# Optimization experiments

Hardware: AMD Instinct MI355X
Metric: run time of the kernel (lower is better)

## Reference

```python
import jax, jax.numpy as jnp
import numpy as np

N = 4096      # nodes
IN = 512      # input_size
D = 128       # output_size per head
H = 4         # num_heads
SLOPE = 0.2   # leaky relu negative slope
NEG = -1e30   # masked-out logit value (finite to keep softmax grad-safe)


def setup_inputs() -> dict:
    key = jax.random.key(0)
    ks = jax.random.split(key, 8)
    stdv = 1.0 / np.sqrt(H * D)
    inputs = jax.random.normal(ks[0], (N, IN), jnp.float32)
    adjacency = jax.random.randint(ks[1], (N, N), 0, 2).astype(jnp.float32)  # dense 0/1 mask
    weight = jax.random.uniform(ks[2], (IN, H * D), jnp.float32, -stdv, stdv)
    weight_u = jax.random.uniform(ks[3], (H, D, 1), jnp.float32, -1.0, 1.0)
    weight_v = jax.random.uniform(ks[4], (H, D, 1), jnp.float32, -1.0, 1.0)
    bias = jax.random.uniform(ks[5], (1, H * D), jnp.float32, -stdv, stdv)
    proj_w = jax.random.normal(ks[6], (IN, H * D), jnp.float32) * 0.02
    proj_b = jnp.zeros((H * D,), jnp.float32)
    return {"inputs": inputs, "adjacency": adjacency, "weight": weight,
            "weight_u": weight_u, "weight_v": weight_v, "bias": bias,
            "proj_w": proj_w, "proj_b": proj_b}


def reference(inputs, adjacency, weight, weight_u, weight_v, bias, proj_w, proj_b):
    # support: [H, N, D]
    support = (inputs @ weight).reshape(N, H, D).transpose(1, 0, 2)
    # f1: per-source scores [H, 1, N]; f2: per-dest scores [H, N, 1]
    f1 = jnp.einsum('hnd,hdo->hn', support, weight_u)[:, None, :]
    f2 = jnp.einsum('hnd,hdo->hn', support, weight_v)[:, :, None]
    logits = f1 + f2                                  # [H, N, N]
    w = jnp.where(logits >= 0, logits, SLOPE * logits)  # leaky_relu
    masked = w * adjacency[None]                      # [H, N, N]
    # torch to_sparse keeps nonzero entries; sparse softmax treats the rest as -inf
    mask = masked != 0
    z = jnp.where(mask, masked, NEG)
    attn = jax.nn.softmax(z, axis=-1) * mask          # rows with no edges -> all zeros
    out = jnp.einsum('hij,hjd->hid', attn, support)   # [H, N, D]
    out = out.transpose(1, 0, 2).reshape(N, H * D)
    out = out + bias
    out = out + inputs @ proj_w + proj_b              # residual projection
    return out
```

## Files before the change

### kernel.cpp

```cpp
#include <hip/hip_runtime.h>

#define NN 4096
#define IND 512
#define HD 512
#define NH 4
#define DH 128
#define K3 1536

typedef __attribute__((ext_vector_type(8))) short bf16x8;
typedef __attribute__((ext_vector_type(4))) float f32x4;
typedef __attribute__((ext_vector_type(4))) unsigned short us4;
typedef __attribute__((ext_vector_type(8))) unsigned short us8;

typedef __attribute__((address_space(3))) void lds_void;
typedef const __attribute__((address_space(1))) void glob_void;

__device__ __forceinline__ void gll16(const void* g, void* l) {
  __builtin_amdgcn_global_load_lds((glob_void*)g, (lds_void*)l, 16, 0, 0);
}

__device__ __forceinline__ unsigned short f2bf(float x) {
  union { float f; unsigned u; } a; a.f = x;
  unsigned r = a.u + 0x7FFFu + ((a.u >> 16) & 1u);
  return (unsigned short)(r >> 16);
}
__device__ __forceinline__ float bf2f(unsigned short b) {
  union { float f; unsigned u; } a; a.u = ((unsigned)b) << 16;
  return a.f;
}

__global__ __launch_bounds__(256) void prep_inputs(const float* __restrict__ x,
                                                   unsigned short* __restrict__ A3) {
  int idx = blockIdx.x * 256 + threadIdx.x;
  int n = idx >> 9, c = idx & 511;
  float v = x[idx];
  unsigned short hi = f2bf(v);
  unsigned short lo = f2bf(v - bf2f(hi));
  size_t base = (size_t)n * K3;
  A3[base + c] = hi;
  A3[base + 512 + c] = hi;
  A3[base + 1024 + c] = lo;
}

__global__ __launch_bounds__(256) void prep_weights(const float* __restrict__ w,
                                                    const float* __restrict__ pw,
                                                    unsigned short* __restrict__ B3T,
                                                    unsigned short* __restrict__ PhT) {
  int idx = blockIdx.x * 256 + threadIdx.x;
  int c = idx >> 9, k = idx & 511;
  float v = w[(size_t)k * HD + c];
  unsigned short hi = f2bf(v);
  unsigned short lo = f2bf(v - bf2f(hi));
  size_t base = (size_t)c * K3;
  B3T[base + k] = hi;
  B3T[base + 512 + k] = lo;
  B3T[base + 1024 + k] = hi;
  float p = pw[(size_t)k * HD + c];
  PhT[(size_t)c * IND + k] = f2bf(p);
}

__global__ __launch_bounds__(256) void gemm_kernel(
    const unsigned short* __restrict__ A3, const unsigned short* __restrict__ B3T,
    const unsigned short* __restrict__ PhT,
    float* __restrict__ support, unsigned short* __restrict__ ST,
    float* __restrict__ resid,
    const float* __restrict__ projb, const float* __restrict__ bias) {
  const int z = blockIdx.z;
  const unsigned short* Bp = z ? PhT : B3T;
  const int ldb = z ? IND : K3;
  const int K = z ? IND : K3;
  const int m0 = blockIdx.x * 128;
  const int n0 = blockIdx.y * 64;
  const int tid = threadIdx.x;
  const int lane = tid & 63;
  const int wv = tid >> 6;
  const int wm = wv & 1, wn = wv >> 1;

  __shared__ unsigned short As[2][128 * 32];
  __shared__ unsigned short Bs[2][64 * 32];

  f32x4 acc[4][2];
#pragma unroll
  for (int a = 0; a < 4; ++a)
#pragma unroll
    for (int b = 0; b < 2; ++b) acc[a][b] = (f32x4){0.f, 0.f, 0.f, 0.f};

  auto STAGE = [&](int buf, int k0) {
#pragma unroll
    for (int s = 0; s < 2; ++s) {
      int c = s * 256 + tid;
      int rr = c >> 2, ko = c & 3;
      gll16(A3 + (size_t)(m0 + rr) * K3 + k0 + ko * 8, &As[buf][c * 8]);
    }
    {
      int c = tid;
      int rr = c >> 2, ko = c & 3;
      gll16(Bp + (size_t)(n0 + rr) * ldb + k0 + ko * 8, &Bs[buf][c * 8]);
    }
  };

  STAGE(0, 0);
  __syncthreads();

  const int lrow = lane & 15;
  const int lkb = (lane >> 4) * 8;
  int buf = 0;
  for (int k0 = 0; k0 < K; k0 += 32) {
    if (k0 + 32 < K) STAGE(buf ^ 1, k0 + 32);
    bf16x8 af[4], bfr[2];
#pragma unroll
    for (int mf = 0; mf < 4; ++mf)
      af[mf] = *(const bf16x8*)(&As[buf][(wm * 64 + mf * 16 + lrow) * 32 + lkb]);
#pragma unroll
    for (int nf = 0; nf < 2; ++nf)
      bfr[nf] = *(const bf16x8*)(&Bs[buf][(wn * 32 + nf * 16 + lrow) * 32 + lkb]);
#pragma unroll
    for (int mf = 0; mf < 4; ++mf)
#pragma unroll
      for (int nf = 0; nf < 2; ++nf)
        acc[mf][nf] = __builtin_amdgcn_mfma_f32_16x16x32_bf16(af[mf], bfr[nf], acc[mf][nf], 0, 0, 0);
    __syncthreads();
    buf ^= 1;
  }

  const int lrow4 = (lane >> 4) * 4;
  const int lcol = lane & 15;
  if (z == 0) {
#pragma unroll
    for (int mf = 0; mf < 4; ++mf) {
#pragma unroll
      for (int nf = 0; nf < 2; ++nf) {
        int rg = m0 + wm * 64 + mf * 16 + lrow4;
        int cg = n0 + wn * 32 + nf * 16 + lcol;
#pragma unroll
        for (int q = 0; q < 4; ++q)
          support[(size_t)(rg + q) * HD + cg] = acc[mf][nf][q];
        us4 st4;
#pragma unroll
        for (int q = 0; q < 4; ++q) st4[q] = f2bf(acc[mf][nf][q]);
        *(us4*)(ST + (size_t)cg * NN + rg) = st4;
      }
    }
  } else {
#pragma unroll
    for (int mf = 0; mf < 4; ++mf) {
#pragma unroll
      for (int nf = 0; nf < 2; ++nf) {
        int rg = m0 + wm * 64 + mf * 16 + lrow4;
        int cg = n0 + wn * 32 + nf * 16 + lcol;
        float addv = projb[cg] + bias[cg];
#pragma unroll
        for (int q = 0; q < 4; ++q)
          resid[(size_t)(rg + q) * HD + cg] = acc[mf][nf][q] + addv;
      }
    }
  }
}

__global__ __launch_bounds__(256) void f1f2_kernel(const float* __restrict__ support,
                                                   const float* __restrict__ wu,
                                                   const float* __restrict__ wv,
                                                   float* __restrict__ g1,
                                                   float* __restrict__ g2) {
  int lane = threadIdx.x & 63;
  int n = blockIdx.x * 4 + (threadIdx.x >> 6);
  const float* srow = support + (size_t)n * HD + lane * 8;
  int h = lane >> 4;
  int d0 = (lane * 8) & 127;
  const float* u = wu + h * DH + d0;
  const float* v = wv + h * DH + d0;
  float du = 0.f, dv = 0.f;
#pragma unroll
  for (int e = 0; e < 8; ++e) {
    float s = srow[e];
    du += s * u[e];
    dv += s * v[e];
  }
#pragma unroll
  for (int off = 1; off < 16; off <<= 1) {
    du += __shfl_xor(du, off);
    dv += __shfl_xor(dv, off);
  }
  if ((lane & 15) == 0) {
    const float L2E = 1.4426950408889634f;
    g1[h * NN + n] = du * L2E;
    g2[h * NN + n] = dv * L2E;
  }
}

__global__ __launch_bounds__(256) void ballot_kernel(const float* __restrict__ adj,
                                                     unsigned long long* __restrict__ bm) {
  int i = blockIdx.x;
  int tid = threadIdx.x, lane = tid & 63, wv = tid >> 6;
  const float* arow = adj + (size_t)i * NN;
#pragma unroll 4
  for (int it = 0; it < 16; ++it) {
    int j = it * 256 + tid;
    unsigned long long b = __ballot(arow[j] != 0.0f);
    if (lane == 0) bm[(size_t)i * 64 + it * 4 + wv] = b;
  }
}

__global__ __launch_bounds__(256) void attn_kernel(
    const unsigned short* __restrict__ ST,
    const unsigned long long* __restrict__ bm,
    const float* __restrict__ g1, const float* __restrict__ g2,
    float* __restrict__ P, float* __restrict__ S) {
  const int bx = blockIdx.x;
  const int by = blockIdx.y;
  const int bz = blockIdx.z;
  const int tid = threadIdx.x;
  const int lane = tid & 63;
  const int w = tid >> 6;

  __shared__ unsigned short tile[2][128 * 32];
  __shared__ unsigned long long bml[32 * 64];
  __shared__ float g1l[2048];

  {
    const unsigned long long* bsrc = bm + (size_t)bx * 64 * 64 + bz * 32;
#pragma unroll
    for (int s = 0; s < 8; ++s) {
      int idx = s * 256 + tid;
      int r = idx >> 5, wi = idx & 31;
      bml[wi * 64 + r] = bsrc[(size_t)r * 64 + wi];
    }
    const float* gsrc = g1 + by * NN + bz * 2048;
#pragma unroll
    for (int s = 0; s < 2; ++s) {
      int idx = s * 256 + tid;
      *(f32x4*)(g1l + idx * 4) = *(const f32x4*)(gsrc + idx * 4);
    }
  }

  const int il = lane & 15;
  const int kg = lane >> 4;
  const int r = w * 16 + il;
  const int ig = bx * 64 + r;
  const float g2v = g2[by * NN + ig];
  const float g2v5 = 0.2f * g2v;
  const unsigned short* stbase = ST + (size_t)by * 128 * NN + bz * 2048;

  auto STAGE = [&](int buf, int jt) {
#pragma unroll
    for (int s = 0; s < 2; ++s) {
      int c = s * 256 + tid;
      int d = c >> 2, jq = c & 3;
      gll16(stbase + (size_t)d * NN + jt + jq * 8, &tile[buf][c * 8]);
    }
  };

  STAGE(0, 0);
  __syncthreads();

  bf16x8 ones;
#pragma unroll
  for (int e = 0; e < 8; ++e) ones[e] = (short)0x3F80;

  f32x4 acc[8];
#pragma unroll
  for (int d = 0; d < 8; ++d) acc[d] = (f32x4){0.f, 0.f, 0.f, 0.f};
  f32x4 asum = (f32x4){0.f, 0.f, 0.f, 0.f};

  union F8 { f32x4 v[2]; float f[8]; };
  const char* bmlB = (const char*)bml;
  int buf = 0;

  for (int jt = 0; jt < 2048; jt += 32) {
    if (jt + 32 < 2048) STAGE(buf ^ 1, jt + 32);

    int b = (jt >> 3) + kg;
    unsigned mby = (unsigned char)bmlB[((b >> 3) * 64 + r) * 8 + (b & 7)];

    F8 gc;
    gc.v[0] = *(const f32x4*)(g1l + jt + kg * 8);
    gc.v[1] = *(const f32x4*)(g1l + jt + kg * 8 + 4);

    bf16x8 bc[8];
#pragma unroll
    for (int d = 0; d < 8; ++d)
      bc[d] = *(const bf16x8*)(&tile[buf][(il + d * 16) * 32 + kg * 8]);

    float p[8];
#pragma unroll
    for (int e = 0; e < 8; ++e) {
      float a = gc.f[e] + g2v;
      float bb = __builtin_fmaf(0.2f, gc.f[e], g2v5);
      float m = fmaxf(a, bb);
      float pe = __builtin_amdgcn_exp2f(m);
      int sext = -(int)((mby >> e) & 1u);
      union { float f; unsigned u; } pu; pu.f = pe;
      pu.u &= (unsigned)sext;
      p[e] = pu.f;
    }

    union { unsigned u[4]; bf16x8 v; } af;
#pragma unroll
    for (int e2 = 0; e2 < 4; ++e2) {
      unsigned pk;
      asm("v_cvt_pk_bf16_f32 %0, %1, %2" : "=v"(pk) : "v"(p[2 * e2]), "v"(p[2 * e2 + 1]));
      af.u[e2] = pk;
    }

#pragma unroll
    for (int d = 0; d < 8; ++d)
      acc[d] = __builtin_amdgcn_mfma_f32_16x16x32_bf16(af.v, bc[d], acc[d], 0, 0, 0);
    asum = __builtin_amdgcn_mfma_f32_16x16x32_bf16(af.v, ones, asum, 0, 0, 0);

    __syncthreads();
    buf ^= 1;
  }

  float* Pp = P + (size_t)bz * NN * HD;
#pragma unroll
  for (int d = 0; d < 8; ++d) {
    int cg = by * 128 + d * 16 + il;
#pragma unroll
    for (int q = 0; q < 4; ++q) {
      int rg = bx * 64 + w * 16 + kg * 4 + q;
      Pp[(size_t)rg * HD + cg] = acc[d][q];
    }
  }
  if (il == 0) {
#pragma unroll
    for (int q = 0; q < 4; ++q) {
      int rg = bx * 64 + w * 16 + kg * 4 + q;
      S[((size_t)bz * 4 + by) * NN + rg] = asum[q];
    }
  }
}

__global__ __launch_bounds__(256) void merge_kernel(const float* __restrict__ P,
                                                    const float* __restrict__ S,
                                                    const float* __restrict__ resid,
                                                    float* __restrict__ out) {
  int idx = blockIdx.x * 256 + threadIdx.x;
  int i = idx >> 7;
  int c = (idx & 127) * 4;
  int h = c >> 7;
  f32x4 v0 = *(const f32x4*)(P + (size_t)i * HD + c);
  f32x4 v1 = *(const f32x4*)(P + (size_t)(NN + i) * HD + c);
  float s = S[(size_t)h * NN + i] + S[(size_t)(4 + h) * NN + i];
  float rs = s > 0.0f ? 1.0f / s : 0.0f;
  f32x4 rr = *(const f32x4*)(resid + (size_t)i * HD + c);
  f32x4 o;
#pragma unroll
  for (int q = 0; q < 4; ++q) o[q] = (v0[q] + v1[q]) * rs + rr[q];
  *(f32x4*)(out + (size_t)i * HD + c) = o;
}

extern "C" void kernel_launch(void* const* d_in, const int* in_sizes, int n_in,
                              void* d_out, int out_size, void* d_ws, size_t ws_size,
                              hipStream_t stream) {
  const float* inputs = (const float*)d_in[0];
  const float* adj = (const float*)d_in[1];
  const float* weight = (const float*)d_in[2];
  const float* wu = (const float*)d_in[3];
  const float* wv = (const float*)d_in[4];
  const float* bias = (const float*)d_in[5];
  const float* projw = (const float*)d_in[6];
  const float* projb = (const float*)d_in[7];
  float* out = (float*)d_out;

  char* ws = (char*)d_ws;
  size_t off = 0;
  unsigned short* A3 = (unsigned short*)(ws + off); off += (size_t)NN * K3 * 2;
  unsigned short* B3T = (unsigned short*)(ws + off); off += (size_t)HD * K3 * 2;
  unsigned short* PhT = (unsigned short*)(ws + off); off += (size_t)HD * IND * 2;
  float* support = (float*)(ws + off); off += (size_t)NN * HD * 4;
  unsigned short* ST = (unsigned short*)(ws + off); off += (size_t)HD * NN * 2;
  float* resid = (float*)(ws + off); off += (size_t)NN * HD * 4;
  float* g1 = (float*)(ws + off); off += (size_t)NH * NN * 4;
  float* g2 = (float*)(ws + off); off += (size_t)NH * NN * 4;
  unsigned long long* bm = (unsigned long long*)(ws + off); off += (size_t)NN * 64 * 8;

  float* P = (float*)(ws + 0);
  float* S = (float*)(ws + (size_t)17 * 1024 * 1024);

  prep_inputs<<<(NN * IND) / 256, 256, 0, stream>>>(inputs, A3);
  prep_weights<<<(IND * HD) / 256, 256, 0, stream>>>(weight, projw, B3T, PhT);
  gemm_kernel<<<dim3(32, 8, 2), 256, 0, stream>>>(A3, B3T, PhT, support, ST, resid, projb, bias);
  f1f2_kernel<<<NN / 4, 256, 0, stream>>>(support, wu, wv, g1, g2);
  ballot_kernel<<<NN, 256, 0, stream>>>(adj, bm);
  attn_kernel<<<dim3(64, 4, 2), 256, 0, stream>>>(ST, bm, g1, g2, P, S);
  merge_kernel<<<2048, 256, 0, stream>>>(P, S, resid, out);
}
```

Baseline: 220.0 us.

## Swizzle GEMM LDS tiles and load attention B-operand directly into registers

The GEMM kernel now XOR-swizzles the k-chunk position per row pair when staging A and B tiles into LDS and reading them back, to reduce LDS bank conflicts on the fragment reads. The attention kernel drops its LDS tile staging and per-iteration __syncthreads. Each lane instead loads its support-transpose fragments straight from global memory into registers, double-buffered across two register sets. This cuts LDS traffic and barriers but raises register pressure and makes each wave issue its own uncoalesced-ish global loads that are duplicated across waves.

```diff
diff --git a/kernel.cpp b/kernel.cpp
--- a/kernel.cpp
+++ b/kernel.cpp
@@ -89,12 +89,14 @@
 #pragma unroll
     for (int s = 0; s < 2; ++s) {
       int c = s * 256 + tid;
-      int rr = c >> 2, ko = c & 3;
+      int rr = c >> 2, sl = c & 3;
+      int ko = sl ^ ((rr >> 1) & 3);
       gll16(A3 + (size_t)(m0 + rr) * K3 + k0 + ko * 8, &As[buf][c * 8]);
     }
     {
       int c = tid;
-      int rr = c >> 2, ko = c & 3;
+      int rr = c >> 2, sl = c & 3;
+      int ko = sl ^ ((rr >> 1) & 3);
       gll16(Bp + (size_t)(n0 + rr) * ldb + k0 + ko * 8, &Bs[buf][c * 8]);
     }
   };
@@ -103,17 +105,23 @@
   __syncthreads();
 
   const int lrow = lane & 15;
-  const int lkb = (lane >> 4) * 8;
+  const int kgc = lane >> 4;
   int buf = 0;
   for (int k0 = 0; k0 < K; k0 += 32) {
     if (k0 + 32 < K) STAGE(buf ^ 1, k0 + 32);
     bf16x8 af[4], bfr[2];
 #pragma unroll
-    for (int mf = 0; mf < 4; ++mf)
-      af[mf] = *(const bf16x8*)(&As[buf][(wm * 64 + mf * 16 + lrow) * 32 + lkb]);
-#pragma unroll
-    for (int nf = 0; nf < 2; ++nf)
-      bfr[nf] = *(const bf16x8*)(&Bs[buf][(wn * 32 + nf * 16 + lrow) * 32 + lkb]);
+    for (int mf = 0; mf < 4; ++mf) {
+      int arow = wm * 64 + mf * 16 + lrow;
+      int asl = kgc ^ ((arow >> 1) & 3);
+      af[mf] = *(const bf16x8*)(&As[buf][arow * 32 + asl * 8]);
+    }
+#pragma unroll
+    for (int nf = 0; nf < 2; ++nf) {
+      int brow = wn * 32 + nf * 16 + lrow;
+      int bsl = kgc ^ ((brow >> 1) & 3);
+      bfr[nf] = *(const bf16x8*)(&Bs[buf][brow * 32 + bsl * 8]);
+    }
 #pragma unroll
     for (int mf = 0; mf < 4; ++mf)
 #pragma unroll
@@ -213,7 +221,6 @@
   const int lane = tid & 63;
   const int w = tid >> 6;
 
-  __shared__ unsigned short tile[2][128 * 32];
   __shared__ unsigned long long bml[32 * 64];
   __shared__ float g1l[2048];
 
@@ -222,8 +229,8 @@
 #pragma unroll
     for (int s = 0; s < 8; ++s) {
       int idx = s * 256 + tid;
-      int r = idx >> 5, wi = idx & 31;
-      bml[wi * 64 + r] = bsrc[(size_t)r * 64 + wi];
+      int wd = idx & 31, r = idx >> 5;
+      bml[wd * 64 + r] = bsrc[(size_t)r * 64 + wd];
     }
     const float* gsrc = g1 + by * NN + bz * 2048;
 #pragma unroll
@@ -239,18 +246,8 @@
   const int ig = bx * 64 + r;
   const float g2v = g2[by * NN + ig];
   const float g2v5 = 0.2f * g2v;
-  const unsigned short* stbase = ST + (size_t)by * 128 * NN + bz * 2048;
-
-  auto STAGE = [&](int buf, int jt) {
-#pragma unroll
-    for (int s = 0; s < 2; ++s) {
-      int c = s * 256 + tid;
-      int d = c >> 2, jq = c & 3;
-      gll16(stbase + (size_t)d * NN + jt + jq * 8, &tile[buf][c * 8]);
-    }
-  };
-
-  STAGE(0, 0);
+  const unsigned short* stp = ST + (size_t)(by * 128 + il) * NN + bz * 2048 + kg * 8;
+
   __syncthreads();
 
   bf16x8 ones;
@@ -262,54 +259,59 @@
   for (int d = 0; d < 8; ++d) acc[d] = (f32x4){0.f, 0.f, 0.f, 0.f};
   f32x4 asum = (f32x4){0.f, 0.f, 0.f, 0.f};
 
-  union F8 { f32x4 v[2]; float f[8]; };
   const char* bmlB = (const char*)bml;
-  int buf = 0;
-
-  for (int jt = 0; jt < 2048; jt += 32) {
-    if (jt + 32 < 2048) STAGE(buf ^ 1, jt + 32);
-
-    int b = (jt >> 3) + kg;
-    unsigned mby = (unsigned char)bmlB[((b >> 3) * 64 + r) * 8 + (b & 7)];
-
-    F8 gc;
-    gc.v[0] = *(const f32x4*)(g1l + jt + kg * 8);
-    gc.v[1] = *(const f32x4*)(g1l + jt + kg * 8 + 4);
-
-    bf16x8 bc[8];
-#pragma unroll
-    for (int d = 0; d < 8; ++d)
-      bc[d] = *(const bf16x8*)(&tile[buf][(il + d * 16) * 32 + kg * 8]);
-
-    float p[8];
-#pragma unroll
-    for (int e = 0; e < 8; ++e) {
-      float a = gc.f[e] + g2v;
-      float bb = __builtin_fmaf(0.2f, gc.f[e], g2v5);
-      float m = fmaxf(a, bb);
-      float pe = __builtin_amdgcn_exp2f(m);
-      int sext = -(int)((mby >> e) & 1u);
-      union { float f; unsigned u; } pu; pu.f = pe;
-      pu.u &= (unsigned)sext;
-      p[e] = pu.f;
-    }
-
-    union { unsigned u[4]; bf16x8 v; } af;
-#pragma unroll
-    for (int e2 = 0; e2 < 4; ++e2) {
-      unsigned pk;
-      asm("v_cvt_pk_bf16_f32 %0, %1, %2" : "=v"(pk) : "v"(p[2 * e2]), "v"(p[2 * e2 + 1]));
-      af.u[e2] = pk;
-    }
-
-#pragma unroll
-    for (int d = 0; d < 8; ++d)
-      acc[d] = __builtin_amdgcn_mfma_f32_16x16x32_bf16(af.v, bc[d], acc[d], 0, 0, 0);
-    asum = __builtin_amdgcn_mfma_f32_16x16x32_bf16(af.v, ones, asum, 0, 0, 0);
-
-    __syncthreads();
-    buf ^= 1;
-  }
+
+  bf16x8 st0[8], st1[8];
+#pragma unroll
+  for (int d = 0; d < 8; ++d) st0[d] = *(const bf16x8*)(stp + (size_t)d * 16 * NN);
+
+#define COMPUTE(SREG, JT)                                                        \
+  {                                                                              \
+    int b = ((JT) >> 3) + kg;                                                    \
+    unsigned mby = (unsigned char)bmlB[((b >> 3) * 64 + r) * 8 + (b & 7)];       \
+    union F8 { f32x4 v[2]; float f[8]; } gc;                                     \
+    gc.v[0] = *(const f32x4*)(g1l + (JT) + kg * 8);                              \
+    gc.v[1] = *(const f32x4*)(g1l + (JT) + kg * 8 + 4);                          \
+    float p[8];                                                                  \
+    _Pragma("unroll")                                                            \
+    for (int e = 0; e < 8; ++e) {                                                \
+      float a = gc.f[e] + g2v;                                                   \
+      float bb = __builtin_fmaf(0.2f, gc.f[e], g2v5);                            \
+      float m = fmaxf(a, bb);                                                    \
+      float pe = __builtin_amdgcn_exp2f(m);                                      \
+      int sext = -(int)((mby >> e) & 1u);                                        \
+      union { float f; unsigned u; } pu; pu.f = pe;                              \
+      pu.u &= (unsigned)sext;                                                    \
+      p[e] = pu.f;                                                               \
+    }                                                                            \
+    union { unsigned u[4]; bf16x8 v; } af;                                       \
+    _Pragma("unroll")                                                            \
+    for (int e2 = 0; e2 < 4; ++e2) {                                             \
+      unsigned pk;                                                               \
+      asm("v_cvt_pk_bf16_f32 %0, %1, %2" : "=v"(pk) : "v"(p[2*e2]), "v"(p[2*e2+1])); \
+      af.u[e2] = pk;                                                             \
+    }                                                                            \
+    _Pragma("unroll")                                                            \
+    for (int d = 0; d < 8; ++d)                                                  \
+      acc[d] = __builtin_amdgcn_mfma_f32_16x16x32_bf16(af.v, SREG[d], acc[d], 0, 0, 0); \
+    asum = __builtin_amdgcn_mfma_f32_16x16x32_bf16(af.v, ones, asum, 0, 0, 0);   \
+  }
+
+  for (int jt = 0; jt < 2048; jt += 64) {
+    {
+      int jn = (jt + 32) & 2047;
+#pragma unroll
+      for (int d = 0; d < 8; ++d) st1[d] = *(const bf16x8*)(stp + (size_t)d * 16 * NN + jn);
+      COMPUTE(st0, jt)
+    }
+    {
+      int jn = (jt + 64) & 2047;
+#pragma unroll
+      for (int d = 0; d < 8; ++d) st0[d] = *(const bf16x8*)(stp + (size_t)d * 16 * NN + jn);
+      COMPUTE(st1, jt + 32)
+    }
+  }
+#undef COMPUTE
 
   float* Pp = P + (size_t)bz * NN * HD;
 #pragma unroll
```

After: 287.3 us. 30.6% more time.
